# Optimization experiments

Hardware: AMD Instinct MI355X
Metric: run time of the kernel (lower is better)

The kernel has to match this reference:

```python
import jax, jax.numpy as jnp
import numpy as np
from jax import lax

# encoder config from the module: (out_ch, kernel, stride), 3x3, padding=1 (pytlib ConvolutionStack)
_LAYERS = [(3, 3, 2), (16, 3, 2), (64, 3, 1), (128, 3, 2), (256, 3, 1)]
_DN = ('NCHW', 'OIHW', 'NCHW')


def _make_params(key):
    params = []
    in_ch = 3
    for i, (out_ch, k, _s) in enumerate(_LAYERS):
        kw, kb = jax.random.split(jax.random.fold_in(key, i))
        fan_in = in_ch * k * k
        W = jax.random.normal(kw, (out_ch, in_ch, k, k), jnp.float32) * np.sqrt(2.0 / fan_in)
        b = jnp.zeros((out_ch,), jnp.float32)
        params.append((W, b))
        in_ch = out_ch
    return params


def _encoder(x, W0, b0, W1, b1, W2, b2, W3, b3, W4, b4):
    Ws = (W0, W1, W2, W3, W4)
    bs = (b0, b1, b2, b3, b4)
    for i, (_oc, _k, s) in enumerate(_LAYERS):
        x = lax.conv_general_dilated(x, Ws[i], (s, s), ((1, 1), (1, 1)), dimension_numbers=_DN)
        x = x + bs[i][None, :, None, None]
        if i < len(_LAYERS) - 1:  # final_relu=False
            x = jax.nn.relu(x)
    return x


def setup_inputs() -> dict:
    key = jax.random.key(0)
    k1, k2, kp = jax.random.split(key, 3)
    crop = jax.random.normal(k1, (64, 3, 64, 64), jnp.float32)
    frame = jax.random.normal(k2, (64, 3, 256, 256), jnp.float32)
    params = _make_params(kp)
    out = {'crop': crop, 'frame': frame}
    for i, (W, b) in enumerate(params):
        out[f'W{i}'] = W
        out[f'b{i}'] = b
    out['gamma'] = jnp.ones((1,), jnp.float32)
    out['beta'] = jnp.zeros((1,), jnp.float32)
    return out


def reference(crop, frame, W0, b0, W1, b1, W2, b2, W3, b3, W4, b4, gamma, beta):
    crop_fm = _encoder(crop, W0, b0, W1, b1, W2, b2, W3, b3, W4, b4)   # [B,256,8,8]
    frame_fm = _encoder(frame, W0, b0, W1, b1, W2, b2, W3, b3, W4, b4)  # [B,256,32,32]

    # per-sample cross-correlation: crop feature map is the conv kernel (vectorized over batch)
    def xcorr(f, k):  # f:[C,H,W], k:[C,h,w] -> [1,Hr,Wr]
        return lax.conv_general_dilated(f[None], k[None], (1, 1), 'VALID', dimension_numbers=_DN)[0]

    rmap = jax.vmap(xcorr)(frame_fm, crop_fm)  # [B,1,25,25]

    # BatchNorm2d(1), training mode: batch stats over (N,H,W), biased variance, eps=1e-5
    mean = jnp.mean(rmap, axis=(0, 2, 3), keepdims=True)
    var = jnp.mean(jnp.square(rmap - mean), axis=(0, 2, 3), keepdims=True)
    rmap = (rmap - mean) * lax.rsqrt(var + 1e-5)
    rmap = rmap * gamma[None, :, None, None] + beta[None, :, None, None]
    return rmap
```

## Files before the change

### kernel.cpp

```cpp
#include <hip/hip_runtime.h>


typedef __bf16 bf16x8 __attribute__((ext_vector_type(8)));
typedef float f32x4 __attribute__((ext_vector_type(4)));
typedef float f32x16 __attribute__((ext_vector_type(16)));
typedef unsigned int u32x4 __attribute__((ext_vector_type(4)));
typedef unsigned int u32x2 __attribute__((ext_vector_type(2)));
typedef unsigned short u16;

#define AS1 __attribute__((address_space(1)))
#define AS3 __attribute__((address_space(3)))

__device__ __forceinline__ u16 f2bf(float v) {
    unsigned u = __float_as_uint(v);
    u += 0x7fffu + ((u >> 16) & 1u);
    return (u16)(u >> 16);
}

__device__ __forceinline__ bf16x8 ldb8(const u16* p) {
    return *(const bf16x8*)p;
}

__device__ __forceinline__ bf16x8 zerob8() {
    u32x4 z = {0u, 0u, 0u, 0u};
    bf16x8 r;
    __builtin_memcpy(&r, &z, 16);
    return r;
}

__device__ __forceinline__ void gload16(const u16* g, u16* l) {
    __builtin_amdgcn_global_load_lds((const AS1 void*)g, (AS3 void*)l, 16, 0, 0);
}

template<int N> __device__ __forceinline__ void wait_vm() {
    asm volatile("s_waitcnt vmcnt(%0)" :: "i"(N) : "memory");
}

__device__ __forceinline__ void bar_mem() {
    asm volatile("" ::: "memory");
    __builtin_amdgcn_s_barrier();
    asm volatile("" ::: "memory");
}

__device__ __forceinline__ int xcd_logical() {
    const int nb = (int)gridDim.x;
    return ((int)blockIdx.x & 7) * (nb >> 3) + ((int)blockIdx.x >> 3);
}

struct CP { const u16* in; u16* out; int IWp, inSS, OWsh, OWpo, outSS, npt; };
struct CQ { const u16* in; u16* out; int IWp, inSS, HWsh, OWsh, OWpo, outSS, pad_o; };

struct HZd { unsigned long long ptr; int B, Hp, Wpx, w8, cum; };
struct HZall { HZd d[8]; int total; };

__device__ __forceinline__ void packone(const float* W, u16* Wp, int idx,
                                        int ICsh, int Kpad)
{
    const int k = idx % Kpad, oc = idx / Kpad;
    const int tap = k >> ICsh, ic = k & ((1 << ICsh) - 1);
    const float v = (tap < 9) ? W[((size_t)(oc << ICsh) + ic) * 9 + tap] : 0.f;
    Wp[idx] = f2bf(v);
}

__global__ __launch_bounds__(256)
void prep_k(HZall h,
            const float* __restrict__ W1, const float* __restrict__ W2,
            const float* __restrict__ W3, const float* __restrict__ W4,
            u16* __restrict__ Wc1, u16* __restrict__ Wp2,
            u16* __restrict__ Wp3, u16* __restrict__ Wp4)
{
    if (blockIdx.x < 1484) {
        const int i = blockIdx.x * 256 + threadIdx.x;
        if (i < 1024) {
            const int k = i & 63, oc = i >> 6;
            const int ky = k >> 4, kx = (k >> 2) & 3, ic = k & 3;
            const float v = (ky < 3 && kx < 3 && ic < 3) ? W1[oc * 27 + ic * 9 + ky * 3 + kx] : 0.f;
            Wc1[i] = f2bf(v);
        } else if (i < 11264) {
            packone(W2, Wp2, i - 1024, 4, 160);
        } else if (i < 84992) {
            packone(W3, Wp3, i - 11264, 6, 576);
        } else if (i < 379904) {
            packone(W4, Wp4, i - 84992, 7, 1152);
        }
        return;
    }
    const int nblk = gridDim.x - 1484;
    for (int i = (blockIdx.x - 1484) * 256 + threadIdx.x; i < h.total; i += nblk * 256) {
        int di = 0;
        #pragma unroll
        for (int j = 1; j < 8; ++j) if (i >= h.d[j].cum) di = j;
        const HZd D = h.d[di];
        const int loc = i - D.cum;
        const int w = loc % D.w8; int t2 = loc / D.w8;
        const int bord = 2 * D.Wpx + 2 * (D.Hp - 2);
        const int pb = t2 % bord; const int b = t2 / bord;
        int oh, ow;
        if (pb < D.Wpx)            { oh = 0;        ow = pb; }
        else if (pb < 2 * D.Wpx)   { oh = D.Hp - 1; ow = pb - D.Wpx; }
        else { const int q = pb - 2 * D.Wpx; oh = 1 + (q >> 1); ow = (q & 1) ? (D.Wpx - 1) : 0; }
        ((unsigned long long*)D.ptr)[((size_t)b * D.Hp * D.Wpx + (size_t)oh * D.Wpx + ow) * D.w8 + w] = 0ull;
    }
}

__device__ __forceinline__ void conv0_body(const float* __restrict__ in,
                                           const float* __restrict__ W,
                                           const float* __restrict__ bias,
                                           u16* __restrict__ outP,
                                           int IH, int IW, int OH, int OW, int idx)
{
    const int OW4 = OW >> 2;
    const int OWp = OW + 2, OHp = OH + 2;
    const int ow4 = idx % OW4; int t = idx / OW4;
    const int oh = t % OH;  const int b = t / OH;
    const int owb = ow4 * 4;
    float a0[4], a1[4], a2[4];
    #pragma unroll
    for (int j = 0; j < 4; ++j) { a0[j] = bias[0]; a1[j] = bias[1]; a2[j] = bias[2]; }
    const float* inb = in + (size_t)b * 3 * IH * IW;
    const int xbase = owb * 2 - 1;
    #pragma unroll
    for (int ic = 0; ic < 3; ++ic) {
        const float* ip = inb + (size_t)ic * IH * IW;
        #pragma unroll
        for (int ky = 0; ky < 3; ++ky) {
            const int y = oh * 2 - 1 + ky;
            if ((unsigned)y >= (unsigned)IH) continue;
            const float* rp = ip + (size_t)y * IW;
            float xr[9];
            #pragma unroll
            for (int i2 = 0; i2 < 9; ++i2) {
                const int x = xbase + i2;
                xr[i2] = ((unsigned)x < (unsigned)IW) ? rp[x] : 0.f;
            }
            #pragma unroll
            for (int kx = 0; kx < 3; ++kx) {
                const float w0 = W[0 * 27 + ic * 9 + ky * 3 + kx];
                const float w1 = W[1 * 27 + ic * 9 + ky * 3 + kx];
                const float w2 = W[2 * 27 + ic * 9 + ky * 3 + kx];
                #pragma unroll
                for (int j = 0; j < 4; ++j) {
                    const float xv = xr[2 * j + kx];
                    a0[j] += xv * w0; a1[j] += xv * w1; a2[j] += xv * w2;
                }
            }
        }
    }
    u16* op = outP + (((size_t)b * OHp + oh + 1) * OWp + owb + 1) * 4;
    #pragma unroll
    for (int j = 0; j < 4; ++j) {
        u32x2 pk;
        pk[0] = (unsigned)f2bf(fmaxf(a0[j], 0.f)) | ((unsigned)f2bf(fmaxf(a1[j], 0.f)) << 16);
        pk[1] = (unsigned)f2bf(fmaxf(a2[j], 0.f));
        *(u32x2*)(op + j * 4) = pk;
    }
}

__global__ __launch_bounds__(256)
void conv0m_k(const float* __restrict__ crop, const float* __restrict__ frame,
              const float* __restrict__ W, const float* __restrict__ bias,
              u16* __restrict__ c0b, u16* __restrict__ f0b)
{
    if (blockIdx.x < 64)
        conv0_body(crop, W, bias, c0b, 64, 64, 32, 32, blockIdx.x * 256 + threadIdx.x);
    else
        conv0_body(frame, W, bias, f0b, 256, 256, 128, 128, (blockIdx.x - 64) * 256 + threadIdx.x);
}

__device__ __forceinline__ void conv1g_body(const u16* __restrict__ inP,
                                            const u16* __restrict__ Wc1,
                                            const float* __restrict__ bias,
                                            u16* __restrict__ outP,
                                            int IWp, int inSS, int OWp, int outSS,
                                            int OWsh, int HWsh, int w, int lane)
{
    const int lr = lane & 15, lg = lane >> 4;
    const int pxb = w * 64;
    const int OW = 1 << OWsh;

    const bf16x8 av0 = ldb8(Wc1 + lr * 64 + lg * 8);
    const bf16x8 av1 = ldb8(Wc1 + lr * 64 + 32 + lg * 8);
    const int ky0 = lg >> 1, kxb = (lg & 1) * 2;
    const int ky1 = 2 + (lg >> 1);

    f32x4 acc[4] = {};
    #pragma unroll
    for (int n = 0; n < 4; ++n) {
        const int px = pxb + n * 16 + lr;
        const int b = px >> HWsh;
        const int rem = px & ((1 << HWsh) - 1);
        const int oh = rem >> OWsh, ow = rem & (OW - 1);
        const u16* ib = inP + (size_t)b * inSS + (((size_t)(oh * 2)) * IWp + ow * 2) * 4;
        const bf16x8 bv0 = ldb8(ib + ((size_t)ky0 * IWp + kxb) * 4);
        acc[n] = __builtin_amdgcn_mfma_f32_16x16x32_bf16(av0, bv0, acc[n], 0, 0, 0);
        const bf16x8 bv1 = ldb8(ib + ((size_t)ky1 * IWp + kxb) * 4);
        acc[n] = __builtin_amdgcn_mfma_f32_16x16x32_bf16(av1, bv1, acc[n], 0, 0, 0);
    }

    const float b0 = bias[lg * 4], b1 = bias[lg * 4 + 1],
                b2 = bias[lg * 4 + 2], b3 = bias[lg * 4 + 3];
    #pragma unroll
    for (int n = 0; n < 4; ++n) {
        const int px = pxb + n * 16 + lr;
        const int b = px >> HWsh;
        const int rem = px & ((1 << HWsh) - 1);
        const int oh = rem >> OWsh, ow = rem & (OW - 1);
        const f32x4 a = acc[n];
        u32x2 pk;
        pk[0] = (unsigned)f2bf(fmaxf(a[0] + b0, 0.f)) | ((unsigned)f2bf(fmaxf(a[1] + b1, 0.f)) << 16);
        pk[1] = (unsigned)f2bf(fmaxf(a[2] + b2, 0.f)) | ((unsigned)f2bf(fmaxf(a[3] + b3, 0.f)) << 16);
        u16* op = outP + (size_t)b * outSS + (((size_t)(oh + 1)) * OWp + (ow + 1)) * 16 + lg * 4;
        *(u32x2*)op = pk;
    }
}

__global__ __launch_bounds__(256)
void conv1m_k(const u16* __restrict__ c0b, u16* __restrict__ c1p,
              const u16* __restrict__ f0b, u16* __restrict__ f1p,
              const u16* __restrict__ Wc1, const float* __restrict__ bias)
{
    const int wv = threadIdx.x >> 6, lane = threadIdx.x & 63;
    if (blockIdx.x < 64)
        conv1g_body(c0b, Wc1, bias, c1p, 34, 4624, 18, 5184, 4, 8, blockIdx.x * 4 + wv, lane);
    else
        conv1g_body(f0b, Wc1, bias, f1p, 130, 67600, 66, 69696, 6, 12, (blockIdx.x - 64) * 4 + wv, lane);
}

template<int BM, int BN, int NWM, int NWN, int S>
__global__ __launch_bounds__(512, 4)
void convq3_k(CQ F, CQ C, int splitPt, int nmt_sh,
              const u16* __restrict__ Wp, const float* __restrict__ bias,
              int IC_sh, int nt, int Kpad, int relu, int OCt)
{
    constexpr int AH = BM * 4 / 512;
    constexpr int BH = BN * 4 / 512;
    constexpr int WAIT  = 2 * AH + BH;
    constexpr int TAIL0 = AH + BH;
    constexpr int ASZ = 2 * 2 * BM * 4 * 8;
    constexpr int BSZ = 2 * 2 * BN * 4 * 8;

    __shared__ __align__(16) u16 SM[ASZ + BSZ];
    u16* Ab = SM;
    u16* Bb = SM + ASZ;

    const int lbid = xcd_logical();
    const int mt  = lbid & ((1 << nmt_sh) - 1);
    const int ptg = lbid >> nmt_sh;
    CQ P; int pt;
    if (ptg < splitPt) { P = F; pt = ptg; }
    else               { P = C; pt = ptg - splitPt; }
    const int ocb = mt * BM;

    const int t    = threadIdx.x;
    const int lane = t & 63;
    const int l32  = lane & 31, hi = lane >> 5;
    const int wv   = t >> 6;
    const int wm   = wv / NWN, wn = wv % NWN;

    const int IC = 1 << IC_sh;
    const int OW = 1 << P.OWsh;
    const int HWm = (1 << P.HWsh) - 1;
    const int pxb = pt * BN;

    const u16* apg[2 * AH];
    #pragma unroll
    for (int h = 0; h < 2; ++h)
        #pragma unroll
        for (int i = 0; i < AH; ++i) {
            const int j = i * 512 + t;
            const int row = j >> 2, o = j & 3;
            const int oct = h * 4 + (o ^ ((row ^ (row >> 2)) & 3));
            apg[h * AH + i] = Wp + (size_t)(ocb + row) * Kpad + oct * 8;
        }
    const u16* bpg[2 * BH];
    #pragma unroll
    for (int h = 0; h < 2; ++h)
        #pragma unroll
        for (int i = 0; i < BH; ++i) {
            const int j = i * 512 + t;
            const int row = j >> 2, o = j & 3;
            const int oct = h * 4 + (o ^ ((row ^ (row >> 2)) & 3));
            const int px = pxb + row;
            const int b = px >> P.HWsh;
            const int rem = px & HWm;
            const int oh = rem >> P.OWsh, ow = rem & (OW - 1);
            bpg[h * BH + i] = P.in + (size_t)b * P.inSS
                            + ((size_t)(oh * S) * P.IWp + ow * S) * IC + oct * 8;
        }

    f32x16 acc[2] = {};

    auto STAGE_A = [&](int buf, int h, int kb) {
        u16* dst = Ab + (size_t)((buf * 2 + h) * BM * 4) * 8;
        #pragma unroll
        for (int i = 0; i < AH; ++i)
            gload16(apg[h * AH + i] + kb, dst + (size_t)(i * 512 + t) * 8);
    };
    auto STAGE_B = [&](int buf, int h, int kb) {
        const int tap = kb >> IC_sh;
        const int ky = (tap * 11) >> 5, kx = tap - 3 * ky;
        const size_t off = ((size_t)(ky * P.IWp + kx) << IC_sh) + (kb & (IC - 1));
        u16* dst = Bb + (size_t)((buf * 2 + h) * BN * 4) * 8;
        #pragma unroll
        for (int i = 0; i < BH; ++i)
            gload16(bpg[h * BH + i] + off, dst + (size_t)(i * 512 + t) * 8);
    };

    STAGE_A(0, 0, 0); STAGE_B(0, 0, 0); STAGE_A(0, 1, 0); STAGE_B(0, 1, 0);

    const int rowB = wn * 32 + l32;
    const int swzB = (rowB ^ (rowB >> 2)) & 3;
    const int rowA0 = wm * 64 + l32;
    const int swzA0 = (rowA0 ^ (rowA0 >> 2)) & 3;
    const int rowA1 = rowA0 + 32;
    const int swzA1 = (rowA1 ^ (rowA1 >> 2)) & 3;

    for (int ks = 0; ks < nt; ++ks) {
        const int cur = ks & 1, nxt = cur ^ 1;
        const int kb1 = (ks + 1) * 64;
        const bool pf = (ks + 1 < nt);

        #pragma unroll
        for (int kk = 0; kk < 2; ++kk) {
            if (pf) STAGE_A(nxt, kk, kb1);
            if (pf)            wait_vm<WAIT>();
            else if (kk == 0)  wait_vm<TAIL0>();
            else               wait_vm<0>();
            bar_mem();

            const u16* Abase = Ab + (size_t)((cur * 2 + kk) * BM * 4) * 8;
            const u16* Bbase = Bb + (size_t)((cur * 2 + kk) * BN * 4) * 8;
            const bf16x8 b0  = ldb8(Bbase + (size_t)(rowB * 4 + ((hi)     ^ swzB)) * 8);
            const bf16x8 b1  = ldb8(Bbase + (size_t)(rowB * 4 + ((2 + hi) ^ swzB)) * 8);
            const bf16x8 a00 = ldb8(Abase + (size_t)(rowA0 * 4 + ((hi)     ^ swzA0)) * 8);
            const bf16x8 a10 = ldb8(Abase + (size_t)(rowA1 * 4 + ((hi)     ^ swzA1)) * 8);
            const bf16x8 a01 = ldb8(Abase + (size_t)(rowA0 * 4 + ((2 + hi) ^ swzA0)) * 8);
            const bf16x8 a11 = ldb8(Abase + (size_t)(rowA1 * 4 + ((2 + hi) ^ swzA1)) * 8);
            if (pf) STAGE_B(nxt, kk, kb1);

            __builtin_amdgcn_s_setprio(1);
            acc[0] = __builtin_amdgcn_mfma_f32_32x32x16_bf16(a00, b0, acc[0], 0, 0, 0);
            acc[1] = __builtin_amdgcn_mfma_f32_32x32x16_bf16(a10, b0, acc[1], 0, 0, 0);
            acc[0] = __builtin_amdgcn_mfma_f32_32x32x16_bf16(a01, b1, acc[0], 0, 0, 0);
            acc[1] = __builtin_amdgcn_mfma_f32_32x32x16_bf16(a11, b1, acc[1], 0, 0, 0);
            __builtin_amdgcn_s_setprio(0);
        }
    }

    bar_mem();
    unsigned long long* SM64 = (unsigned long long*)SM;
    const int pxl = wn * 32 + l32;
    const int sw = ((pxl & 3) << 1) | ((pxl >> 2) & 1);
    #pragma unroll
    for (int msub = 0; msub < 2; ++msub) {
        #pragma unroll
        for (int q = 0; q < 4; ++q) {
            const int ocl = wm * 64 + msub * 32 + q * 8 + hi * 4;
            const float b0 = bias[ocb + ocl],     b1 = bias[ocb + ocl + 1],
                        b2 = bias[ocb + ocl + 2], b3 = bias[ocb + ocl + 3];
            float v0 = acc[msub][q * 4 + 0] + b0;
            float v1 = acc[msub][q * 4 + 1] + b1;
            float v2 = acc[msub][q * 4 + 2] + b2;
            float v3 = acc[msub][q * 4 + 3] + b3;
            if (relu) {
                v0 = fmaxf(v0, 0.f); v1 = fmaxf(v1, 0.f);
                v2 = fmaxf(v2, 0.f); v3 = fmaxf(v3, 0.f);
            }
            u32x2 pk;
            pk[0] = (unsigned)f2bf(v0) | ((unsigned)f2bf(v1) << 16);
            pk[1] = (unsigned)f2bf(v2) | ((unsigned)f2bf(v3) << 16);
            const int u8 = (ocl >> 2) ^ (sw << 1);
            *(u32x2*)&SM64[(size_t)pxl * (BM / 4) + u8] = pk;
        }
    }
    bar_mem();
    constexpr int UPX16 = BM / 8;
    constexpr int NIT = BN * UPX16 / 512;
    #pragma unroll
    for (int it = 0; it < NIT; ++it) {
        const int g = it * 512 + t;
        const int px = g / UPX16;
        const int ul = g & (UPX16 - 1);
        const int sw2 = ((px & 3) << 1) | ((px >> 2) & 1);
        const int phys = ul ^ sw2;
        const u32x4 val = *(const u32x4*)&SM[((size_t)px * UPX16 + phys) * 8];
        const int flat = pxb + px;
        const int b = flat >> P.HWsh;
        const int rem = flat & HWm;
        const int oh = rem >> P.OWsh, ow = rem & (OW - 1);
        u16* dst = P.out + (size_t)b * P.outSS
                 + (((size_t)(oh + P.pad_o)) * P.OWpo + (ow + P.pad_o)) * OCt
                 + ocb + ul * 8;
        *(u32x4*)dst = val;
    }
}

template<int BM, int BN, int NWM, int NWN, int S>
__global__ __launch_bounds__(256, 2)
void convg4_k(CP A, CP B, int split,
              const u16* __restrict__ Wp, const float* __restrict__ bias,
              int IC_sh, int pad_o, int Kreal, int nt, int Kpad, int relu, int OCtot)
{
    constexpr int MF = BM / (NWM * 16);
    constexpr int NF = BN / (NWN * 16);
    constexpr int ASLOT = BM * 4;
    constexpr int BSLOT = BN * 4;
    constexpr int AISS = ASLOT / 256;
    constexpr int BISS = BSLOT / 256;
    constexpr int NSTG = AISS + BISS;

    __shared__ __align__(16) u16 Ab[4][ASLOT * 8];
    __shared__ __align__(16) u16 Bb[4][BSLOT * 8];

    const int lbid = xcd_logical();
    CP P; int bid;
    if (lbid < split) { P = A; bid = lbid; }
    else              { P = B; bid = lbid - split; }

    const int t    = threadIdx.x;
    const int wv   = t >> 6, lane = t & 63;
    const int lr   = lane & 15, lg = lane >> 4;
    const int wm   = wv / NWN, wn = wv % NWN;

    const int tilesPerB = (OCtot / BM) * P.npt;
    const int b  = bid / tilesPerB;
    const int r0 = bid - b * tilesPerB;
    const int mt = r0 / P.npt, pt = r0 - mt * P.npt;
    const int ocb = mt * BM, pxb = pt * BN;
    const int IC = 1 << IC_sh;
    const int OW = 1 << P.OWsh;

    const u16* __restrict__ inb = P.in + (size_t)b * P.inSS;

    const u16* agp[AISS];
    #pragma unroll
    for (int i = 0; i < AISS; ++i) {
        const int j = i * 256 + t;
        const int row = j >> 2, c = j & 3;
        const int og = c ^ ((row ^ (row >> 2)) & 3);
        agp[i] = Wp + (size_t)(ocb + row) * Kpad + og * 8;
    }
    const u16* bpx[BISS]; int bog8[BISS];
    #pragma unroll
    for (int i = 0; i < BISS; ++i) {
        const int j = i * 256 + t;
        const int row = j >> 2, c = j & 3;
        const int og = c ^ ((row ^ (row >> 2)) & 3);
        const int px = pxb + row;
        const int oh = px >> P.OWsh, ow = px & (OW - 1);
        bpx[i] = inb + ((size_t)(oh * S) * P.IWp + ow * S) * IC;
        bog8[i] = og * 8;
    }

    f32x4 acc[MF][NF] = {};

    auto STAGE = [&](int buf, int kb) {
        #pragma unroll
        for (int i = 0; i < AISS; ++i)
            gload16(agp[i] + kb, &Ab[buf][(size_t)(i * 256 + t) * 8]);
        #pragma unroll
        for (int i = 0; i < BISS; ++i) {
            const int k = kb + bog8[i];
            const int tap = k >> IC_sh;
            const int ic = k & (IC - 1);
            const int ky = (tap * 11) >> 5, kx = tap - 3 * ky;
            const u16* g = bpx[i] + ((size_t)ky * P.IWp + kx) * IC + ic;
            if (k >= Kreal) g = inb;
            gload16(g, &Bb[buf][(size_t)(i * 256 + t) * 8]);
        }
    };

    STAGE(0, 0);
    if (1 < nt) STAGE(1, 32);
    if (2 < nt) STAGE(2, 64);

    for (int ks = 0; ks < nt; ++ks) {
        const int rem = nt - 1 - ks;
        if (rem >= 2)      wait_vm<2 * NSTG>();
        else if (rem == 1) wait_vm<NSTG>();
        else               wait_vm<0>();
        bar_mem();
        if (ks + 3 < nt) STAGE((ks + 3) & 3, (ks + 3) * 32);

        const int cur = ks & 3;
        bf16x8 af[MF], bf_[NF];
        #pragma unroll
        for (int m = 0; m < MF; ++m) {
            const int row = wm * (MF * 16) + m * 16 + lr;
            const int o = lg ^ ((row ^ (row >> 2)) & 3);
            af[m] = ldb8(&Ab[cur][(size_t)(row * 4 + o) * 8]);
        }
        #pragma unroll
        for (int n = 0; n < NF; ++n) {
            const int row = wn * (NF * 16) + n * 16 + lr;
            const int o = lg ^ ((row ^ (row >> 2)) & 3);
            bf_[n] = ldb8(&Bb[cur][(size_t)(row * 4 + o) * 8]);
        }

        __builtin_amdgcn_s_setprio(1);
        #pragma unroll
        for (int m = 0; m < MF; ++m)
            #pragma unroll
            for (int n = 0; n < NF; ++n)
                acc[m][n] = __builtin_amdgcn_mfma_f32_16x16x32_bf16(af[m], bf_[n], acc[m][n], 0, 0, 0);
        __builtin_amdgcn_s_setprio(0);
    }

    #pragma unroll
    for (int m = 0; m < MF; ++m) {
        const int oc0 = ocb + wm * (MF * 16) + m * 16 + lg * 4;
        const float b0 = bias[oc0], b1 = bias[oc0 + 1], b2 = bias[oc0 + 2], b3 = bias[oc0 + 3];
        #pragma unroll
        for (int n = 0; n < NF; ++n) {
            const int px = pxb + wn * (NF * 16) + n * 16 + lr;
            const int oh = px >> P.OWsh, ow = px & (OW - 1);
            const f32x4 a = acc[m][n];
            float v0 = a[0] + b0, v1 = a[1] + b1, v2 = a[2] + b2, v3 = a[3] + b3;
            if (relu) {
                v0 = fmaxf(v0, 0.f); v1 = fmaxf(v1, 0.f);
                v2 = fmaxf(v2, 0.f); v3 = fmaxf(v3, 0.f);
            }
            u32x2 pk;
            pk[0] = (unsigned)f2bf(v0) | ((unsigned)f2bf(v1) << 16);
            pk[1] = (unsigned)f2bf(v2) | ((unsigned)f2bf(v3) << 16);
            u16* op = P.out + (size_t)b * P.outSS +
                      (((size_t)(oh + pad_o)) * P.OWpo + (ow + pad_o)) * (size_t)OCtot + oc0;
            *(u32x2*)op = pk;
        }
    }
}

__global__ __launch_bounds__(256)
void xcmf_k(const u16* __restrict__ ffm, const u16* __restrict__ cfm,
            float* __restrict__ R)
{
    const int w    = blockIdx.x * 4 + (threadIdx.x >> 6);
    const int lane = threadIdx.x & 63;
    const int lr   = lane & 15, lg = lane >> 4;
    const int b  = w / 25;
    const int tp = w - b * 25;

    const int col0 = tp * 32 + lr;
    const int col1 = col0 + 16;
    const int y0 = col0 / 25, x0 = col0 - y0 * 25;
    const int y1 = col1 / 25, x1 = col1 - y1 * 25;

    const u16* fb = ffm + (size_t)b * 262144;
    const u16* f0 = fb + ((size_t)y0 * 32 + x0) * 256 + lg * 8;
    const u16* f1 = fb + ((size_t)y1 * 32 + x1) * 256 + lg * 8;
    const u16* ab = cfm + (size_t)b * 16384 + (size_t)lr * 2048 + lg * 8;
    const bool arow = (lr < 8);

    f32x4 acc0 = {}, acc1 = {};
    #pragma unroll 4
    for (int kb = 0; kb < 2048; kb += 32) {
        const bf16x8 av = arow ? ldb8(ab + kb) : zerob8();
        const bf16x8 bv0 = ldb8(f0 + kb);
        const bf16x8 bv1 = ldb8(f1 + kb);
        acc0 = __builtin_amdgcn_mfma_f32_16x16x32_bf16(av, bv0, acc0, 0, 0, 0);
        acc1 = __builtin_amdgcn_mfma_f32_16x16x32_bf16(av, bv1, acc1, 0, 0, 0);
    }

    if (lg < 2) {
        float* rb = R + (size_t)b * 6400;
        #pragma unroll
        for (int j = 0; j < 4; ++j) {
            const int d = lg * 4 + j;
            rb[(size_t)d * 800 + col0] = acc0[j];
            rb[(size_t)d * 800 + col1] = acc1[j];
        }
    }
}

__global__ __launch_bounds__(1024)
void bn_k(const float* __restrict__ R, float* __restrict__ part,
          const float* __restrict__ gamma, const float* __restrict__ beta,
          float* __restrict__ out)
{
    const int N = 40000;
    const int tid = threadIdx.x;
    __shared__ float rs[1024], rq[1024];
    __shared__ float mean_s, inv_s;
    float s = 0.f, q = 0.f;
    for (int i = tid; i < N; i += 1024) {
        const int b = i / 625;
        const int o = i - b * 625;
        const float* rb = R + (size_t)b * 6400 + o;
        float v = 0.f;
        #pragma unroll
        for (int d = 0; d < 8; ++d) v += rb[(size_t)d * 800 + d * 25];
        part[i] = v;
        s += v; q += v * v;
    }
    rs[tid] = s; rq[tid] = q;
    __syncthreads();
    for (int off = 512; off > 0; off >>= 1) {
        if (tid < off) { rs[tid] += rs[tid + off]; rq[tid] += rq[tid + off]; }
        __syncthreads();
    }
    if (tid == 0) {
        const float m = rs[0] / (float)N;
        mean_s = m;
        inv_s = rsqrtf(rq[0] / (float)N - m * m + 1e-5f);
    }
    __syncthreads();
    const float g = gamma[0], bt = beta[0];
    for (int i = tid; i < N; i += 1024)
        out[i] = (part[i] - mean_s) * inv_s * g + bt;
}


extern "C" void kernel_launch(void* const* d_in, const int* in_sizes, int n_in,
                              void* d_out, int out_size, void* d_ws, size_t ws_size,
                              hipStream_t stream)
{
    (void)in_sizes; (void)n_in; (void)out_size; (void)ws_size;
    const float* crop  = (const float*)d_in[0];
    const float* frame = (const float*)d_in[1];
    const float* W[5]; const float* bb[5];
    for (int i = 0; i < 5; ++i) { W[i] = (const float*)d_in[2 + 2*i]; bb[i] = (const float*)d_in[3 + 2*i]; }
    const float* gamma = (const float*)d_in[12];
    const float* beta  = (const float*)d_in[13];
    float* out = (float*)d_out;

    unsigned char* ws = (unsigned char*)d_ws;
    u16*   f0b  = (u16*)(ws + 0);
    u16*   f1p  = (u16*)(ws + 8652800);
    u16*   f2p  = (u16*)(ws + 17573888);
    u16*   f3p  = (u16*)(ws + 53258240);
    u16*   ffm  = (u16*)(ws + 0);
    u16*   c0b  = (u16*)(ws + 72198144);
    u16*   c1p  = (u16*)(ws + 72790016);
    u16*   c2p  = (u16*)(ws + 73453568);
    u16*   c3p  = (u16*)(ws + 76107776);
    u16*   cfm  = (u16*)(ws + 77746176);
    u16*   Wc1  = (u16*)(ws + 79843328);
    u16*   Wp2  = (u16*)(ws + 79845376);
    u16*   Wp3  = (u16*)(ws + 79865856);
    u16*   Wp4  = (u16*)(ws + 80013312);
    float* Rbuf = (float*)(ws + 80603136);
    float* part = (float*)(ws + 82241536);

    HZall hz;
    const unsigned long long ptrs[8] = {(unsigned long long)c0b, (unsigned long long)c1p,
        (unsigned long long)c2p, (unsigned long long)c3p, (unsigned long long)f0b,
        (unsigned long long)f1p, (unsigned long long)f2p, (unsigned long long)f3p};
    const int Hps[8] = {34, 18, 18, 10, 130, 66, 66, 34};
    const int w8s[8] = {1, 4, 16, 32, 1, 4, 16, 32};
    int cum = 0;
    for (int i = 0; i < 8; ++i) {
        hz.d[i].ptr = ptrs[i]; hz.d[i].B = 64; hz.d[i].Hp = Hps[i];
        hz.d[i].Wpx = Hps[i]; hz.d[i].w8 = w8s[i]; hz.d[i].cum = cum;
        cum += 64 * (2 * Hps[i] + 2 * (Hps[i] - 2)) * w8s[i];
    }
    hz.total = cum;
    prep_k<<<1856, 256, 0, stream>>>(hz, W[1], W[2], W[3], W[4], Wc1, Wp2, Wp3, Wp4);

    conv0m_k<<<1088, 256, 0, stream>>>(crop, frame, W[0], bb[0], c0b, f0b);
    conv1m_k<<<1088, 256, 0, stream>>>(c0b, c1p, f0b, f1p, Wc1, bb[1]);
    {
        CP Ac = {c1p, c2p, 18,  5184, 4, 18, 20736,  1};
        CP Bf = {f1p, f2p, 66, 69696, 6, 66, 278784, 16};
        convg4_k<64,256,1,4,1><<<1088, 256, 0, stream>>>(Ac, Bf, 64, Wp2, bb[2],
            4, 1, 144, 5, 160, 1, 64);
    }

    {
        CQ F3 = {f2p, f3p, 66, 278784, 10,  5,   34,  147968, 1};
        CQ C3 = {c2p, c3p, 18,  20736,  6,  3,   10,   12800, 1};
        convq3_k<128,128,2,4,2><<< 544, 512, 0, stream>>>(F3, C3, 512, 0, Wp3, bb[3], 6,  9,  576, 1, 128);
        CQ F4 = {f3p, ffm, 34, 147968, 10,  5,   32,  262144, 0};
        CQ C4 = {c3p, cfm, 10,  12800,  6,  3,    8,   16384, 0};
        convq3_k<128,128,2,4,1><<<1088, 512, 0, stream>>>(F4, C4, 512, 1, Wp4, bb[4], 7, 18, 1152, 0, 256);
    }

    xcmf_k<<<400, 256, 0, stream>>>(ffm, cfm, Rbuf);
    bn_k<<<1, 1024, 0, stream>>>(Rbuf, part, gamma, beta, out);
}
```

Baseline: 229.0 us.

## Use 4 waves with 64x64 warp tiles in conv3/conv4 implicit GEMM

Replaces the 8-wave (512-thread) conv kernel, where each wave computed a 64x32 sub-tile, with a 4-wave (256-thread) variant where each wave computes a 64x64 sub-tile holding a 2x2 set of MFMA accumulators. Each wave now reuses its A and B fragments across twice as many MFMAs, cutting LDS reads per FLOP. Each thread also issues twice as many global-to-LDS loads. In exchange, register pressure per wave rises and fewer waves are resident to hide latency.

```diff
diff --git a/kernel.cpp b/kernel.cpp
--- a/kernel.cpp
+++ b/kernel.cpp
@@ -226,14 +226,14 @@
         conv1g_body(f0b, Wc1, bias, f1p, 130, 67600, 66, 69696, 6, 12, (blockIdx.x - 64) * 4 + wv, lane);
 }
 
-template<int BM, int BN, int NWM, int NWN, int S>
-__global__ __launch_bounds__(512, 4)
-void convq3_k(CQ F, CQ C, int splitPt, int nmt_sh,
+template<int BM, int BN, int S>
+__global__ __launch_bounds__(256, 2)
+void convq4_k(CQ F, CQ C, int splitPt, int nmt_sh,
               const u16* __restrict__ Wp, const float* __restrict__ bias,
               int IC_sh, int nt, int Kpad, int relu, int OCt)
 {
-    constexpr int AH = BM * 4 / 512;
-    constexpr int BH = BN * 4 / 512;
+    constexpr int AH = BM * 4 / 256;
+    constexpr int BH = BN * 4 / 256;
     constexpr int WAIT  = 2 * AH + BH;
     constexpr int TAIL0 = AH + BH;
     constexpr int ASZ = 2 * 2 * BM * 4 * 8;
@@ -255,7 +255,7 @@
     const int lane = t & 63;
     const int l32  = lane & 31, hi = lane >> 5;
     const int wv   = t >> 6;
-    const int wm   = wv / NWN, wn = wv % NWN;
+    const int wm   = wv >> 1, wn = wv & 1;
 
     const int IC = 1 << IC_sh;
     const int OW = 1 << P.OWsh;
@@ -267,7 +267,7 @@
     for (int h = 0; h < 2; ++h)
         #pragma unroll
         for (int i = 0; i < AH; ++i) {
-            const int j = i * 512 + t;
+            const int j = i * 256 + t;
             const int row = j >> 2, o = j & 3;
             const int oct = h * 4 + (o ^ ((row ^ (row >> 2)) & 3));
             apg[h * AH + i] = Wp + (size_t)(ocb + row) * Kpad + oct * 8;
@@ -277,7 +277,7 @@
     for (int h = 0; h < 2; ++h)
         #pragma unroll
         for (int i = 0; i < BH; ++i) {
-            const int j = i * 512 + t;
+            const int j = i * 256 + t;
             const int row = j >> 2, o = j & 3;
             const int oct = h * 4 + (o ^ ((row ^ (row >> 2)) & 3));
             const int px = pxb + row;
@@ -288,13 +288,13 @@
                             + ((size_t)(oh * S) * P.IWp + ow * S) * IC + oct * 8;
         }
 
-    f32x16 acc[2] = {};
+    f32x16 acc[2][2] = {};
 
     auto STAGE_A = [&](int buf, int h, int kb) {
         u16* dst = Ab + (size_t)((buf * 2 + h) * BM * 4) * 8;
         #pragma unroll
         for (int i = 0; i < AH; ++i)
-            gload16(apg[h * AH + i] + kb, dst + (size_t)(i * 512 + t) * 8);
+            gload16(apg[h * AH + i] + kb, dst + (size_t)(i * 256 + t) * 8);
     };
     auto STAGE_B = [&](int buf, int h, int kb) {
         const int tap = kb >> IC_sh;
@@ -303,17 +303,19 @@
         u16* dst = Bb + (size_t)((buf * 2 + h) * BN * 4) * 8;
         #pragma unroll
         for (int i = 0; i < BH; ++i)
-            gload16(bpg[h * BH + i] + off, dst + (size_t)(i * 512 + t) * 8);
+            gload16(bpg[h * BH + i] + off, dst + (size_t)(i * 256 + t) * 8);
     };
 
     STAGE_A(0, 0, 0); STAGE_B(0, 0, 0); STAGE_A(0, 1, 0); STAGE_B(0, 1, 0);
 
-    const int rowB = wn * 32 + l32;
-    const int swzB = (rowB ^ (rowB >> 2)) & 3;
-    const int rowA0 = wm * 64 + l32;
-    const int swzA0 = (rowA0 ^ (rowA0 >> 2)) & 3;
-    const int rowA1 = rowA0 + 32;
-    const int swzA1 = (rowA1 ^ (rowA1 >> 2)) & 3;
+    int rowA[2], swzA[2], rowB[2], swzB[2];
+    #pragma unroll
+    for (int s2 = 0; s2 < 2; ++s2) {
+        rowA[s2] = wm * 64 + s2 * 32 + l32;
+        swzA[s2] = (rowA[s2] ^ (rowA[s2] >> 2)) & 3;
+        rowB[s2] = wn * 64 + s2 * 32 + l32;
+        swzB[s2] = (rowB[s2] ^ (rowB[s2] >> 2)) & 3;
+    }
 
     for (int ks = 0; ks < nt; ++ks) {
         const int cur = ks & 1, nxt = cur ^ 1;
@@ -330,55 +332,63 @@
 
             const u16* Abase = Ab + (size_t)((cur * 2 + kk) * BM * 4) * 8;
             const u16* Bbase = Bb + (size_t)((cur * 2 + kk) * BN * 4) * 8;
-            const bf16x8 b0  = ldb8(Bbase + (size_t)(rowB * 4 + ((hi)     ^ swzB)) * 8);
-            const bf16x8 b1  = ldb8(Bbase + (size_t)(rowB * 4 + ((2 + hi) ^ swzB)) * 8);
-            const bf16x8 a00 = ldb8(Abase + (size_t)(rowA0 * 4 + ((hi)     ^ swzA0)) * 8);
-            const bf16x8 a10 = ldb8(Abase + (size_t)(rowA1 * 4 + ((hi)     ^ swzA1)) * 8);
-            const bf16x8 a01 = ldb8(Abase + (size_t)(rowA0 * 4 + ((2 + hi) ^ swzA0)) * 8);
-            const bf16x8 a11 = ldb8(Abase + (size_t)(rowA1 * 4 + ((2 + hi) ^ swzA1)) * 8);
+            bf16x8 af[2][2], bf_[2][2];
+            #pragma unroll
+            for (int s2 = 0; s2 < 2; ++s2)
+                #pragma unroll
+                for (int kp = 0; kp < 2; ++kp) {
+                    af[s2][kp]  = ldb8(Abase + (size_t)(rowA[s2] * 4 + ((kp * 2 + hi) ^ swzA[s2])) * 8);
+                    bf_[s2][kp] = ldb8(Bbase + (size_t)(rowB[s2] * 4 + ((kp * 2 + hi) ^ swzB[s2])) * 8);
+                }
             if (pf) STAGE_B(nxt, kk, kb1);
 
             __builtin_amdgcn_s_setprio(1);
-            acc[0] = __builtin_amdgcn_mfma_f32_32x32x16_bf16(a00, b0, acc[0], 0, 0, 0);
-            acc[1] = __builtin_amdgcn_mfma_f32_32x32x16_bf16(a10, b0, acc[1], 0, 0, 0);
-            acc[0] = __builtin_amdgcn_mfma_f32_32x32x16_bf16(a01, b1, acc[0], 0, 0, 0);
-            acc[1] = __builtin_amdgcn_mfma_f32_32x32x16_bf16(a11, b1, acc[1], 0, 0, 0);
+            #pragma unroll
+            for (int kp = 0; kp < 2; ++kp)
+                #pragma unroll
+                for (int m = 0; m < 2; ++m)
+                    #pragma unroll
+                    for (int n = 0; n < 2; ++n)
+                        acc[m][n] = __builtin_amdgcn_mfma_f32_32x32x16_bf16(af[m][kp], bf_[n][kp], acc[m][n], 0, 0, 0);
             __builtin_amdgcn_s_setprio(0);
         }
     }
 
     bar_mem();
     unsigned long long* SM64 = (unsigned long long*)SM;
-    const int pxl = wn * 32 + l32;
-    const int sw = ((pxl & 3) << 1) | ((pxl >> 2) & 1);
-    #pragma unroll
-    for (int msub = 0; msub < 2; ++msub) {
-        #pragma unroll
-        for (int q = 0; q < 4; ++q) {
-            const int ocl = wm * 64 + msub * 32 + q * 8 + hi * 4;
-            const float b0 = bias[ocb + ocl],     b1 = bias[ocb + ocl + 1],
-                        b2 = bias[ocb + ocl + 2], b3 = bias[ocb + ocl + 3];
-            float v0 = acc[msub][q * 4 + 0] + b0;
-            float v1 = acc[msub][q * 4 + 1] + b1;
-            float v2 = acc[msub][q * 4 + 2] + b2;
-            float v3 = acc[msub][q * 4 + 3] + b3;
-            if (relu) {
-                v0 = fmaxf(v0, 0.f); v1 = fmaxf(v1, 0.f);
-                v2 = fmaxf(v2, 0.f); v3 = fmaxf(v3, 0.f);
+    #pragma unroll
+    for (int n = 0; n < 2; ++n) {
+        const int pxl = wn * 64 + n * 32 + l32;
+        const int sw = ((pxl & 3) << 1) | ((pxl >> 2) & 1);
+        #pragma unroll
+        for (int m = 0; m < 2; ++m) {
+            #pragma unroll
+            for (int q = 0; q < 4; ++q) {
+                const int ocl = wm * 64 + m * 32 + q * 8 + hi * 4;
+                const float b0 = bias[ocb + ocl],     b1 = bias[ocb + ocl + 1],
+                            b2 = bias[ocb + ocl + 2], b3 = bias[ocb + ocl + 3];
+                float v0 = acc[m][n][q * 4 + 0] + b0;
+                float v1 = acc[m][n][q * 4 + 1] + b1;
+                float v2 = acc[m][n][q * 4 + 2] + b2;
+                float v3 = acc[m][n][q * 4 + 3] + b3;
+                if (relu) {
+                    v0 = fmaxf(v0, 0.f); v1 = fmaxf(v1, 0.f);
+                    v2 = fmaxf(v2, 0.f); v3 = fmaxf(v3, 0.f);
+                }
+                u32x2 pk;
+                pk[0] = (unsigned)f2bf(v0) | ((unsigned)f2bf(v1) << 16);
+                pk[1] = (unsigned)f2bf(v2) | ((unsigned)f2bf(v3) << 16);
+                const int u8 = (ocl >> 2) ^ (sw << 1);
+                *(u32x2*)&SM64[(size_t)pxl * (BM / 4) + u8] = pk;
             }
-            u32x2 pk;
-            pk[0] = (unsigned)f2bf(v0) | ((unsigned)f2bf(v1) << 16);
-            pk[1] = (unsigned)f2bf(v2) | ((unsigned)f2bf(v3) << 16);
-            const int u8 = (ocl >> 2) ^ (sw << 1);
-            *(u32x2*)&SM64[(size_t)pxl * (BM / 4) + u8] = pk;
         }
     }
     bar_mem();
     constexpr int UPX16 = BM / 8;
-    constexpr int NIT = BN * UPX16 / 512;
+    constexpr int NIT = BN * UPX16 / 256;
     #pragma unroll
     for (int it = 0; it < NIT; ++it) {
-        const int g = it * 512 + t;
+        const int g = it * 256 + t;
         const int px = g / UPX16;
         const int ul = g & (UPX16 - 1);
         const int sw2 = ((px & 3) << 1) | ((px >> 2) & 1);
@@ -668,10 +678,10 @@
     {
         CQ F3 = {f2p, f3p, 66, 278784, 10,  5,   34,  147968, 1};
         CQ C3 = {c2p, c3p, 18,  20736,  6,  3,   10,   12800, 1};
-        convq3_k<128,128,2,4,2><<< 544, 512, 0, stream>>>(F3, C3, 512, 0, Wp3, bb[3], 6,  9,  576, 1, 128);
+        convq4_k<128,128,2><<< 544, 256, 0, stream>>>(F3, C3, 512, 0, Wp3, bb[3], 6,  9,  576, 1, 128);
         CQ F4 = {f3p, ffm, 34, 147968, 10,  5,   32,  262144, 0};
         CQ C4 = {c3p, cfm, 10,  12800,  6,  3,    8,   16384, 0};
-        convq3_k<128,128,2,4,1><<<1088, 512, 0, stream>>>(F4, C4, 512, 1, Wp4, bb[4], 7, 18, 1152, 0, 256);
+        convq4_k<128,128,1><<<1088, 256, 0, stream>>>(F4, C4, 512, 1, Wp4, bb[4], 7, 18, 1152, 0, 256);
     }
 
     xcmf_k<<<400, 256, 0, stream>>>(ffm, cfm, Rbuf);
```

New measurement: 232.7 us. About the same (+1.6%).
